# Kernel tuning notes

Hardware: AMD Instinct MI355X
Metric: run time of the kernel (lower is better)

Reference implementation:

```python
import jax, jax.numpy as jnp
import numpy as np
from jax import lax

TEMP = 0.05
MOMENTUM = 0.9
EPS = 1e-12


def _l2_normalize(x, axis=-1):
    n = jnp.sqrt(jnp.sum(x * x, axis=axis, keepdims=True))
    return x / jnp.maximum(n, EPS)


def _cross_entropy(logits, targets):
    # mean over batch of -log_softmax(logits)[target]
    logp = jax.nn.log_softmax(logits, axis=-1)
    return -jnp.mean(jnp.take_along_axis(logp, targets[:, None], axis=-1))


def _momentum_update(features, x, targets, m):
    # Sequential per-sample read-modify-write (faithful to the torch loop,
    # matters when targets contain duplicates). carry = memory bank.
    def step(f, xy):
        x_i, y_i = xy
        row = m * f[y_i] + (1.0 - m) * x_i
        row = row / jnp.linalg.norm(row)
        return f.at[y_i].set(row), None
    f, _ = lax.scan(step, features, (x, targets))
    return f


def setup_inputs() -> dict:
    key = jax.random.key(0)
    k1, k2, k3, k4, k5, k6 = jax.random.split(key, 6)
    B, D, N = 512, 1024, 16384
    inputs_rgb = jax.random.normal(k1, (B, D), dtype=jnp.float32)
    inputs_ir = jax.random.normal(k2, (B, D), dtype=jnp.float32)
    targets_rgb = jax.random.randint(k3, (B,), 0, N, dtype=jnp.int32)
    targets_ir = jax.random.randint(k4, (B,), 0, N, dtype=jnp.int32)
    # memory banks (buffers); initialized as normalized random rows to mimic a
    # warmed-up cluster memory (the module starts at zeros, degenerate for CE)
    features_rgb = _l2_normalize(jax.random.normal(k5, (N, D), dtype=jnp.float32))
    features_ir = _l2_normalize(jax.random.normal(k6, (N, D), dtype=jnp.float32))
    return {"inputs_rgb": inputs_rgb, "inputs_ir": inputs_ir,
            "targets_rgb": targets_rgb, "targets_ir": targets_ir,
            "features_rgb": features_rgb, "features_ir": features_ir}


def reference(inputs_rgb, inputs_ir, targets_rgb, targets_ir, features_rgb, features_ir):
    x_rgb = _l2_normalize(inputs_rgb)  # [B, D]
    x_ir = _l2_normalize(inputs_ir)
    logits_rgb = (x_rgb @ features_rgb.T) / TEMP  # [B, N]
    logits_ir = (x_ir @ features_ir.T) / TEMP
    loss_rgb = _cross_entropy(logits_rgb, targets_rgb)
    loss_ir = _cross_entropy(logits_ir, targets_ir)
    # side-effect of CM.backward in the original: momentum scatter update + renorm
    # (change_scale == 1.0 so the Hungarian cross-modal exchange is skipped)
    new_features_rgb = _momentum_update(features_rgb, x_rgb, targets_rgb, MOMENTUM)
    new_features_ir = _momentum_update(features_ir, x_ir, targets_ir, MOMENTUM)
    return (loss_rgb, loss_ir, new_features_rgb, new_features_ir)
```

## Files before the change

### kernel.cpp

```cpp
#include <hip/hip_runtime.h>
#include <math.h>

#define BATCH 512
#define DIM   1024
#define NCLUS 16384
#define TINV  20.0f

typedef __attribute__((ext_vector_type(4))) float f32x4;
typedef __attribute__((ext_vector_type(2))) float f32x2;
typedef __attribute__((ext_vector_type(8))) short bf16x8;

static __device__ __forceinline__ unsigned short f2bf(float f) {
  unsigned int u = __float_as_uint(f);
  u += 0x7FFFu + ((u >> 16) & 1u);
  return (unsigned short)(u >> 16);
}

typedef const __attribute__((address_space(1))) unsigned int* gas1_t;
typedef __attribute__((address_space(3))) unsigned int* las3_t;
static __device__ __forceinline__ void gload16(const void* g, void* l) {
  __builtin_amdgcn_global_load_lds((gas1_t)g, (las3_t)l, 16, 0, 0);
}

__global__ void nrm_kernel(const float* __restrict__ in_rgb,
                           const float* __restrict__ in_ir,
                           float* __restrict__ xf,
                           unsigned short* __restrict__ xb,
                           float* __restrict__ accum) {
  int gid = blockIdx.x * blockDim.x + threadIdx.x;
  if (gid < 2048) accum[gid] = 0.0f;

  int row = blockIdx.x;
  int mod = row >> 9;
  int r   = row & 511;
  const float* in = (mod ? in_ir : in_rgb) + (size_t)r * DIM;
  float* xo          = xf + ((size_t)mod * BATCH + r) * DIM;
  unsigned short* xbo = xb + ((size_t)mod * BATCH + r) * DIM;

  int t = threadIdx.x;
  float4 v = ((const float4*)in)[t];
  float ss = v.x*v.x + v.y*v.y + v.z*v.z + v.w*v.w;
#pragma unroll
  for (int m = 1; m < 64; m <<= 1) ss += __shfl_xor(ss, m, 64);
  __shared__ float red[4];
  if ((t & 63) == 0) red[t >> 6] = ss;
  __syncthreads();
  float inv = 1.0f / fmaxf(sqrtf(red[0] + red[1] + red[2] + red[3]), 1e-12f);
  float4 o = make_float4(v.x * inv, v.y * inv, v.z * inv, v.w * inv);
  ((float4*)xo)[t] = o;
  ushort4 ob = make_ushort4(f2bf(o.x), f2bf(o.y), f2bf(o.z), f2bf(o.w));
  ((ushort4*)xbo)[t] = ob;
}

#define BM 128
#define BN 128
#define BK 32
#define KT_N (DIM / BK)

__launch_bounds__(256, 4)
__global__ void gemm_lse_kernel(const unsigned short* __restrict__ xb,
                                const float* __restrict__ f_rgb,
                                const float* __restrict__ f_ir,
                                const int* __restrict__ t_rgb,
                                const int* __restrict__ t_ir,
                                float* __restrict__ outc,
                                float* __restrict__ rowsum,
                                float* __restrict__ tgtlog) {
  const int nt  = blockIdx.x;
  const int bt  = blockIdx.y & 3;
  const int mod = blockIdx.y >> 2;

  const unsigned short* X = xb + ((size_t)mod * BATCH + bt * BM) * DIM;
  const float* Ff = (mod ? f_ir : f_rgb) + (size_t)nt * BN * DIM;
  const float* Fq = Ff + (size_t)bt * 32 * DIM;
  float* Oq = outc + ((size_t)mod * NCLUS + (size_t)nt * BN + bt * 32) * DIM;
  const int* tg = mod ? t_ir : t_rgb;
  float* rs = rowsum + mod * BATCH;
  float* tl = tgtlog + mod * BATCH;

  __shared__ __align__(16) unsigned short As[2][BM * BK];
  __shared__ __align__(16) unsigned short Bs[2][BN * BK];

  const int tid  = threadIdx.x;
  const int wid  = tid >> 6;
  const int lane = tid & 63;
  const int wr = wid >> 1, wc = wid & 1;
  const int l15 = lane & 15, lhi = lane >> 4;
  const int sw = (l15 & 6) << 3;

  f32x4 acc[4][4];
#pragma unroll
  for (int m = 0; m < 4; ++m)
#pragma unroll
    for (int n = 0; n < 4; ++n) acc[m][n] = (f32x4){0.f, 0.f, 0.f, 0.f};

  auto A_STAGE = [&](int buf, int kt) {
#pragma unroll
    for (int c = 0; c < 2; ++c) {
      int q = c * 256 + tid;
      int cs = (q & 3) ^ ((q >> 3) & 3);
      gload16(X + (size_t)(q >> 2) * DIM + kt * BK + cs * 8,
              &As[buf][(c * 256 + wid * 64) * 8]);
    }
  };
  auto B_LOAD = [&](f32x4* br, int kk) {
#pragma unroll
    for (int c = 0; c < 2; ++c) {
      int h = c * 256 + tid, row = h >> 2, j = h & 3;
      const float* sp = Ff + (size_t)row * DIM + kk + j * 8;
      br[c * 2]     = *(const f32x4*)sp;
      br[c * 2 + 1] = *(const f32x4*)(sp + 4);
    }
  };
  auto B_WRITE = [&](int buf, const f32x4* br) {
#pragma unroll
    for (int c = 0; c < 2; ++c) {
      int h = c * 256 + tid, row = h >> 2, j = h & 3;
      union { bf16x8 v; unsigned int w[4]; } p;
      const unsigned int* x0 = (const unsigned int*)&br[c * 2];
      const unsigned int* x1 = (const unsigned int*)&br[c * 2 + 1];
      p.w[0] = (x0[0] >> 16) | (x0[1] & 0xFFFF0000u);
      p.w[1] = (x0[2] >> 16) | (x0[3] & 0xFFFF0000u);
      p.w[2] = (x1[0] >> 16) | (x1[1] & 0xFFFF0000u);
      p.w[3] = (x1[2] >> 16) | (x1[3] & 0xFFFF0000u);
      *(bf16x8*)((char*)&Bs[buf][0] + row * 64 + ((j ^ ((row >> 1) & 3)) << 4)) = p.v;
    }
  };
  auto LDA = [&](int buf, int row) {
    return *(const bf16x8*)((const char*)As[buf] + ((row * 64 + lhi * 16) ^ sw));
  };
  auto LDB = [&](int buf, int row) {
    return *(const bf16x8*)((const char*)Bs[buf] + ((row * 64 + lhi * 16) ^ sw));
  };
  auto COMPUTE = [&](int buf) {
    bf16x8 a[4], b[4];
#pragma unroll
    for (int n = 0; n < 4; ++n) b[n] = LDB(buf, wc * 64 + n * 16 + l15);
#pragma unroll
    for (int m = 0; m < 4; ++m) a[m] = LDA(buf, wr * 64 + m * 16 + l15);
#pragma unroll
    for (int m = 0; m < 4; ++m)
#pragma unroll
      for (int n = 0; n < 4; ++n)
        acc[m][n] = __builtin_amdgcn_mfma_f32_16x16x32_bf16(a[m], b[n], acc[m][n], 0, 0, 0);
  };

  {
    f32x4 br0[4];
    B_LOAD(br0, 0);
    A_STAGE(0, 0);
    B_WRITE(0, br0);
  }
  __syncthreads();

  for (int s = 0; s < KT_N; ++s) {
    const int cur = s & 1;
    const int id = s * 256 + tid;
    const int r32 = id >> 8, col = id & 255;
    f32x4 craw = *((const f32x4*)(Fq + (size_t)r32 * DIM) + col);
    f32x4 braw[4];
    if (s + 1 < KT_N) {
      B_LOAD(braw, (s + 1) * BK);
      A_STAGE(cur ^ 1, s + 1);
    }
    __builtin_amdgcn_sched_barrier(0);
    COMPUTE(cur);
    if (s + 1 < KT_N) B_WRITE(cur ^ 1, braw);
    {
      float* dp = Oq + (size_t)r32 * DIM + (size_t)col * 4;
      __builtin_nontemporal_store((f32x2){craw.x, craw.y}, (f32x2*)dp);
      __builtin_nontemporal_store((f32x2){craw.z, craw.w}, (f32x2*)(dp + 2));
    }
    if (s + 1 < KT_N) {
      asm volatile("s_waitcnt vmcnt(2) lgkmcnt(0)" ::: "memory");
      __builtin_amdgcn_sched_barrier(0);
      __builtin_amdgcn_s_barrier();
    }
  }

#pragma unroll
  for (int m = 0; m < 4; ++m) {
    const int browbase = bt * BM + wr * 64 + m * 16 + lhi * 4;
    float esum[4];
#pragma unroll
    for (int j = 0; j < 4; ++j) {
      const int brow = browbase + j;
      const int t = tg[brow];
      float e = 0.f;
#pragma unroll
      for (int n = 0; n < 4; ++n) {
        float logit = acc[m][n][j] * TINV;
        e += __expf(logit);
        int col = nt * BN + wc * 64 + n * 16 + l15;
        if (col == t) tl[brow] = logit;
      }
      esum[j] = e;
    }
#pragma unroll
    for (int j = 0; j < 4; ++j) {
      float e = esum[j];
      e += __shfl_xor(e, 1, 64);
      e += __shfl_xor(e, 2, 64);
      e += __shfl_xor(e, 4, 64);
      e += __shfl_xor(e, 8, 64);
      if (l15 == 0) atomicAdd(rs + browbase + j, e);
    }
  }
}

__global__ void loss_kernel(const float* __restrict__ rowsum,
                            const float* __restrict__ tgtlog,
                            float* __restrict__ out) {
  int t = threadIdx.x;
  float lr = logf(rowsum[t]) - tgtlog[t];
  float li = logf(rowsum[BATCH + t]) - tgtlog[BATCH + t];
#pragma unroll
  for (int m = 1; m < 64; m <<= 1) { lr += __shfl_xor(lr, m, 64); li += __shfl_xor(li, m, 64); }
  __shared__ float sr[8], si[8];
  if ((t & 63) == 0) { sr[t >> 6] = lr; si[t >> 6] = li; }
  __syncthreads();
  if (t == 0) {
    float a = 0.f, b = 0.f;
#pragma unroll
    for (int i = 0; i < 8; ++i) { a += sr[i]; b += si[i]; }
    out[0] = a * (1.0f / BATCH);
    out[1] = b * (1.0f / BATCH);
  }
}

__global__ void mom_kernel(const int* __restrict__ t_rgb,
                           const int* __restrict__ t_ir,
                           const float* __restrict__ xf,
                           float* __restrict__ out) {
  const int i   = blockIdx.x;
  const int mod = blockIdx.y;
  const int* tg = mod ? t_ir : t_rgb;
  const int y = tg[i];
  for (int j = 0; j < i; ++j)
    if (tg[j] == y) return;

  const float* x = xf + (size_t)mod * BATCH * DIM;
  float* rowp = out + (size_t)mod * NCLUS * DIM + (size_t)y * DIM;

  const int t = threadIdx.x;
  float2 r0 = ((const float2*)rowp)[t];
  float2 r1 = ((const float2*)rowp)[t + 256];
  __shared__ float red[4];

  for (int j = i; j < BATCH; ++j) {
    if (tg[j] != y) continue;
    const float2* xr = (const float2*)(x + (size_t)j * DIM);
    float2 x0 = xr[t], x1 = xr[t + 256];
    r0.x = 0.9f * r0.x + 0.1f * x0.x;
    r0.y = 0.9f * r0.y + 0.1f * x0.y;
    r1.x = 0.9f * r1.x + 0.1f * x1.x;
    r1.y = 0.9f * r1.y + 0.1f * x1.y;
    float ss = r0.x*r0.x + r0.y*r0.y + r1.x*r1.x + r1.y*r1.y;
#pragma unroll
    for (int m = 1; m < 64; m <<= 1) ss += __shfl_xor(ss, m, 64);
    if ((t & 63) == 0) red[t >> 6] = ss;
    __syncthreads();
    float tot = red[0] + red[1] + red[2] + red[3];
    __syncthreads();
    float inv = 1.0f / sqrtf(tot);
    r0.x *= inv; r0.y *= inv; r1.x *= inv; r1.y *= inv;
  }
  ((float2*)rowp)[t] = r0;
  ((float2*)rowp)[t + 256] = r1;
}

extern "C" void kernel_launch(void* const* d_in, const int* in_sizes, int n_in,
                              void* d_out, int out_size, void* d_ws, size_t ws_size,
                              hipStream_t stream) {
  (void)in_sizes; (void)n_in; (void)out_size; (void)ws_size;
  const float* in_rgb = (const float*)d_in[0];
  const float* in_ir  = (const float*)d_in[1];
  const int*   t_rgb  = (const int*)d_in[2];
  const int*   t_ir   = (const int*)d_in[3];
  const float* f_rgb  = (const float*)d_in[4];
  const float* f_ir   = (const float*)d_in[5];
  float* out = (float*)d_out;

  char* ws = (char*)d_ws;
  float*          xf     = (float*)ws;
  unsigned short* xb     = (unsigned short*)(ws + (4u<<20));
  float*          rowsum = (float*)(ws + (6u<<20));
  float*          tgtlog = rowsum + 1024;

  nrm_kernel<<<1024, 256, 0, stream>>>(in_rgb, in_ir, xf, xb, rowsum);
  gemm_lse_kernel<<<dim3(128, 8), 256, 0, stream>>>(xb, f_rgb, f_ir, t_rgb, t_ir,
                                                    out + 2, rowsum, tgtlog);
  mom_kernel<<<dim3(512, 2), 256, 0, stream>>>(t_rgb, t_ir, xf, out + 2);
  loss_kernel<<<1, 512, 0, stream>>>(rowsum, tgtlog, out);
}
```

Baseline: 170.1 us.

## Stage fp32 B tiles directly to LDS via async loads, convert at compute

```diff
diff --git a/kernel.cpp b/kernel.cpp
--- a/kernel.cpp
+++ b/kernel.cpp
@@ -57,7 +57,7 @@
 #define BK 32
 #define KT_N (DIM / BK)
 
-__launch_bounds__(256, 4)
+__launch_bounds__(256, 3)
 __global__ void gemm_lse_kernel(const unsigned short* __restrict__ xb,
                                 const float* __restrict__ f_rgb,
                                 const float* __restrict__ f_ir,
@@ -79,7 +79,7 @@
   float* tl = tgtlog + mod * BATCH;
 
   __shared__ __align__(16) unsigned short As[2][BM * BK];
-  __shared__ __align__(16) unsigned short Bs[2][BN * BK];
+  __shared__ __align__(16) float          Bf[2][BN * BK];
 
   const int tid  = threadIdx.x;
   const int wid  = tid >> 6;
@@ -103,39 +103,37 @@
               &As[buf][(c * 256 + wid * 64) * 8]);
     }
   };
-  auto B_LOAD = [&](f32x4* br, int kk) {
-#pragma unroll
-    for (int c = 0; c < 2; ++c) {
-      int h = c * 256 + tid, row = h >> 2, j = h & 3;
-      const float* sp = Ff + (size_t)row * DIM + kk + j * 8;
-      br[c * 2]     = *(const f32x4*)sp;
-      br[c * 2 + 1] = *(const f32x4*)(sp + 4);
-    }
-  };
-  auto B_WRITE = [&](int buf, const f32x4* br) {
-#pragma unroll
-    for (int c = 0; c < 2; ++c) {
-      int h = c * 256 + tid, row = h >> 2, j = h & 3;
-      union { bf16x8 v; unsigned int w[4]; } p;
-      const unsigned int* x0 = (const unsigned int*)&br[c * 2];
-      const unsigned int* x1 = (const unsigned int*)&br[c * 2 + 1];
-      p.w[0] = (x0[0] >> 16) | (x0[1] & 0xFFFF0000u);
-      p.w[1] = (x0[2] >> 16) | (x0[3] & 0xFFFF0000u);
-      p.w[2] = (x1[0] >> 16) | (x1[1] & 0xFFFF0000u);
-      p.w[3] = (x1[2] >> 16) | (x1[3] & 0xFFFF0000u);
-      *(bf16x8*)((char*)&Bs[buf][0] + row * 64 + ((j ^ ((row >> 1) & 3)) << 4)) = p.v;
+  auto B_STAGE = [&](int buf, int kt) {
+#pragma unroll
+    for (int c = 0; c < 4; ++c) {
+      int q = c * 256 + tid;
+      int row = q >> 3;
+      int cs = (q & 7) ^ (row & 7);
+      gload16(Ff + (size_t)row * DIM + kt * BK + cs * 4,
+              (char*)&Bf[buf][0] + (c * 256 + wid * 64) * 16);
     }
   };
   auto LDA = [&](int buf, int row) {
     return *(const bf16x8*)((const char*)As[buf] + ((row * 64 + lhi * 16) ^ sw));
   };
-  auto LDB = [&](int buf, int row) {
-    return *(const bf16x8*)((const char*)Bs[buf] + ((row * 64 + lhi * 16) ^ sw));
+  auto LDBF = [&](int buf, int row, int h) {
+    return *(const f32x4*)((const char*)&Bf[buf][0] +
+                           row * 128 + ((((lhi << 1) | h) ^ (row & 7)) << 4));
   };
   auto COMPUTE = [&](int buf) {
     bf16x8 a[4], b[4];
 #pragma unroll
-    for (int n = 0; n < 4; ++n) b[n] = LDB(buf, wc * 64 + n * 16 + l15);
+    for (int n = 0; n < 4; ++n) {
+      const int row = wc * 64 + n * 16 + l15;
+      f32x4 r0 = LDBF(buf, row, 0);
+      f32x4 r1 = LDBF(buf, row, 1);
+      union { bf16x8 v; unsigned int w[4]; } p;
+      p.w[0] = (__float_as_uint(r0.x) >> 16) | (__float_as_uint(r0.y) & 0xFFFF0000u);
+      p.w[1] = (__float_as_uint(r0.z) >> 16) | (__float_as_uint(r0.w) & 0xFFFF0000u);
+      p.w[2] = (__float_as_uint(r1.x) >> 16) | (__float_as_uint(r1.y) & 0xFFFF0000u);
+      p.w[3] = (__float_as_uint(r1.z) >> 16) | (__float_as_uint(r1.w) & 0xFFFF0000u);
+      b[n] = p.v;
+    }
 #pragma unroll
     for (int m = 0; m < 4; ++m) a[m] = LDA(buf, wr * 64 + m * 16 + l15);
 #pragma unroll
@@ -145,12 +143,8 @@
         acc[m][n] = __builtin_amdgcn_mfma_f32_16x16x32_bf16(a[m], b[n], acc[m][n], 0, 0, 0);
   };
 
-  {
-    f32x4 br0[4];
-    B_LOAD(br0, 0);
-    A_STAGE(0, 0);
-    B_WRITE(0, br0);
-  }
+  A_STAGE(0, 0);
+  B_STAGE(0, 0);
   __syncthreads();
 
   for (int s = 0; s < KT_N; ++s) {
@@ -158,14 +152,12 @@
     const int id = s * 256 + tid;
     const int r32 = id >> 8, col = id & 255;
     f32x4 craw = *((const f32x4*)(Fq + (size_t)r32 * DIM) + col);
-    f32x4 braw[4];
     if (s + 1 < KT_N) {
-      B_LOAD(braw, (s + 1) * BK);
       A_STAGE(cur ^ 1, s + 1);
+      B_STAGE(cur ^ 1, s + 1);
     }
     __builtin_amdgcn_sched_barrier(0);
     COMPUTE(cur);
-    if (s + 1 < KT_N) B_WRITE(cur ^ 1, braw);
     {
       float* dp = Oq + (size_t)r32 * DIM + (size_t)col * 4;
       __builtin_nontemporal_store((f32x2){craw.x, craw.y}, (f32x2*)dp);
```

Result: slower. 178.8 us (+5.1%).
